# Kernel tuning notes

Hardware: AMD Instinct MI355X
Metric: run time of the kernel (lower is better)

The kernel has to match this reference:

```python
import jax, jax.numpy as jnp
import numpy as np

N_NODES = 100000
N_EDGES = 640000


def _sage_conv(x, src, dst, w_agg, b, w_root, n_nodes):
    # mean aggregation of source features into destination nodes
    msgs = x[src]  # [E, D] gather
    summed = jax.ops.segment_sum(msgs, dst, num_segments=n_nodes)  # [N, D]
    deg = jax.ops.segment_sum(jnp.ones((src.shape[0],), dtype=x.dtype), dst,
                              num_segments=n_nodes)  # [N]
    mean = summed / jnp.clip(deg, 1.0)[:, None]  # isolated nodes -> 0
    # PyG SAGEConv: lin_l(agg) + lin_r(x); bias lives on lin_l
    return mean @ w_agg.T + b + x @ w_root.T


def setup_inputs() -> dict:
    key = jax.random.key(0)
    ks = jax.random.split(key, 8)
    d_in, d_hid, d_out = 128, 256, 64
    x = jax.random.normal(ks[0], (N_NODES, d_in), dtype=jnp.float32)
    edge_index = jax.random.randint(ks[1], (2, N_EDGES), 0, N_NODES, dtype=jnp.int64)
    s = 0.05
    return {
        "x": x,
        "edge_index": edge_index,
        "w1_agg": jax.random.normal(ks[2], (d_hid, d_in), dtype=jnp.float32) * s,
        "b1": jax.random.normal(ks[3], (d_hid,), dtype=jnp.float32) * s,
        "w1_root": jax.random.normal(ks[4], (d_hid, d_in), dtype=jnp.float32) * s,
        "w2_agg": jax.random.normal(ks[5], (d_out, d_hid), dtype=jnp.float32) * s,
        "b2": jax.random.normal(ks[6], (d_out,), dtype=jnp.float32) * s,
        "w2_root": jax.random.normal(ks[7], (d_out, d_hid), dtype=jnp.float32) * s,
    }


def reference(x, edge_index, w1_agg, b1, w1_root, w2_agg, b2, w2_root):
    src, dst = edge_index[0], edge_index[1]
    n = x.shape[0]
    h = _sage_conv(x, src, dst, w1_agg, b1, w1_root, n)
    h = jax.nn.relu(h)
    # dropout(p=0.5) is identity in eval mode
    h = _sage_conv(h, src, dst, w2_agg, b2, w2_root, n)
    return jax.nn.log_softmax(h, axis=1)
```

## Files before the change

### kernel.cpp

```cpp
#include <hip/hip_runtime.h>

#define N_NODES 100000
#define N_EDGES 640000
#define D_IN 128
#define D_HID 256
#define D_OUT 64

#define NROWPAD 100096
#define CAP 32

#define OB_CNT      0u
#define OB_BUCKET   401408u
#define OB_XB       13201408u
#define OB_XQ       38825984u
#define OB_MEANB    51638272u
#define OB_HB       77262848u
#define OB_ZRB      128512000u
#define OB_ZAQ      141324288u
#define OB_WCAT1    147730432u
#define OB_WCAT2    147861504u

typedef __attribute__((ext_vector_type(8))) short bf16x8;
typedef __attribute__((ext_vector_type(8))) ushort ushort8;
typedef __attribute__((ext_vector_type(4))) float f32x4;
typedef __attribute__((ext_vector_type(2))) float f32x2;

__device__ __forceinline__ ushort f2bf(float f) {
    uint u = __float_as_uint(f);
    u += 0x7FFFu + ((u >> 16) & 1u);
    return (ushort)(u >> 16);
}
__device__ __forceinline__ float bf1(ushort u) { return __uint_as_float((uint)u << 16); }
__device__ __forceinline__ uchar f2q(float v) {
    return (uchar)(__builtin_amdgcn_cvt_pk_fp8_f32(v, v, 0, false) & 0xFF);
}
__device__ __forceinline__ uint pk8(float4 v) {
    uint q = (uint)__builtin_amdgcn_cvt_pk_fp8_f32(v.x, v.y, 0, false);
    return (uint)__builtin_amdgcn_cvt_pk_fp8_f32(v.z, v.w, (int)q, true);
}


__global__ __launch_bounds__(256) void k_z(
    int* __restrict__ cnt,
    const float* __restrict__ w1a, const float* __restrict__ w1r,
    const float* __restrict__ w2r, const float* __restrict__ w2a,
    ushort* __restrict__ wcat1, ushort* __restrict__ wcat2)
{
    int b = blockIdx.x;
    if (b < 98) {
        int i = (b * 256 + threadIdx.x) * 4;
        *(int4*)(cnt + i) = make_int4(0, 0, 0, 0);
    } else {
        int i = (b - 98) * 256 + threadIdx.x;
        if (i < 65536) {
            int n = i >> 8, k = i & 255;
            float v = (k < 128) ? w1a[n * 128 + k] : w1r[n * 128 + (k - 128)];
            wcat1[i] = f2bf(v);
        } else {
            int j = i - 65536;
            int n = j >> 8, k = j & 255;
            float v = (n < 64) ? w2r[n * 256 + k] : w2a[(n - 64) * 256 + k];
            wcat2[j] = f2bf(v);
        }
    }
}


__global__ __launch_bounds__(256) void k_fc(
    const int* __restrict__ src, const int* __restrict__ dst,
    int* __restrict__ cnt, int* __restrict__ bucket,
    const float* __restrict__ x, ushort* __restrict__ xb,
    uchar* __restrict__ xq)
{
    int b = blockIdx.x;
    if (b < 625) {
        int e = (b * 256 + threadIdx.x) * 4;
        int4 d = *(const int4*)(dst + e);
        int4 sv = *(const int4*)(src + e);
        int p0 = atomicAdd(&cnt[d.x], 1);
        int p1 = atomicAdd(&cnt[d.y], 1);
        int p2 = atomicAdd(&cnt[d.z], 1);
        int p3 = atomicAdd(&cnt[d.w], 1);
        if (p0 < CAP) bucket[(d.x << 5) + p0] = sv.x;
        if (p1 < CAP) bucket[(d.y << 5) + p1] = sv.y;
        if (p2 < CAP) bucket[(d.z << 5) + p2] = sv.z;
        if (p3 < CAP) bucket[(d.w << 5) + p3] = sv.w;
    } else {
        size_t i = ((size_t)(b - 625) * 256 + threadIdx.x) * 16;
        float4 v0 = *(const float4*)(x + i);
        float4 v1 = *(const float4*)(x + i + 4);
        float4 v2 = *(const float4*)(x + i + 8);
        float4 v3 = *(const float4*)(x + i + 12);
        ushort8 o0, o1;
        o0[0]=f2bf(v0.x); o0[1]=f2bf(v0.y); o0[2]=f2bf(v0.z); o0[3]=f2bf(v0.w);
        o0[4]=f2bf(v1.x); o0[5]=f2bf(v1.y); o0[6]=f2bf(v1.z); o0[7]=f2bf(v1.w);
        o1[0]=f2bf(v2.x); o1[1]=f2bf(v2.y); o1[2]=f2bf(v2.z); o1[3]=f2bf(v2.w);
        o1[4]=f2bf(v3.x); o1[5]=f2bf(v3.y); o1[6]=f2bf(v3.z); o1[7]=f2bf(v3.w);
        *(ushort8*)(xb + i) = o0;
        *(ushort8*)(xb + i + 8) = o1;
        uint4 q;
        q.x = pk8(v0); q.y = pk8(v1); q.z = pk8(v2); q.w = pk8(v3);
        *(uint4*)(xq + i) = q;
    }
}


__global__ __launch_bounds__(256) void k_gather(
    const uchar* __restrict__ xq, const int* __restrict__ cnt,
    const int* __restrict__ bucket, ushort* __restrict__ meanb)
{
    int tid = threadIdx.x;
    int node = blockIdx.x * 8 + (tid >> 5);
    int l = tid & 31;
    int g = l & 3, t = l >> 2;
    int nraw = cnt[node];
    int n = min(nraw, CAP);
    const int* cs = bucket + (node << 5);

    float a[16] = {};
    for (int j = 0; j < n; j += 4) {
        int jj = j + g;
        int ii = (jj < n) ? jj : 0;
        float w = (jj < n) ? 1.0f : 0.0f;
        int s = cs[ii];
        uint4 q = *(const uint4*)(xq + (size_t)s * D_IN + t * 16);
        f32x2 p;
        p = __builtin_amdgcn_cvt_pk_f32_fp8(q.x, false); a[0] += w*p.x; a[1] += w*p.y;
        p = __builtin_amdgcn_cvt_pk_f32_fp8(q.x, true);  a[2] += w*p.x; a[3] += w*p.y;
        p = __builtin_amdgcn_cvt_pk_f32_fp8(q.y, false); a[4] += w*p.x; a[5] += w*p.y;
        p = __builtin_amdgcn_cvt_pk_f32_fp8(q.y, true);  a[6] += w*p.x; a[7] += w*p.y;
        p = __builtin_amdgcn_cvt_pk_f32_fp8(q.z, false); a[8] += w*p.x; a[9] += w*p.y;
        p = __builtin_amdgcn_cvt_pk_f32_fp8(q.z, true);  a[10]+= w*p.x; a[11]+= w*p.y;
        p = __builtin_amdgcn_cvt_pk_f32_fp8(q.w, false); a[12]+= w*p.x; a[13]+= w*p.y;
        p = __builtin_amdgcn_cvt_pk_f32_fp8(q.w, true);  a[14]+= w*p.x; a[15]+= w*p.y;
    }

    float b[8];
    #pragma unroll
    for (int j = 0; j < 8; ++j) {
        int base = (j & 3) + 8 * (j >> 2);
        float mine = (l & 1) ? a[base + 4] : a[base];
        float send = (l & 1) ? a[base]     : a[base + 4];
        b[j] = mine + __shfl_xor(send, 1);
    }
    float c[4];
    #pragma unroll
    for (int j = 0; j < 4; ++j) {
        float mine = (l & 2) ? b[j + 4] : b[j];
        float send = (l & 2) ? b[j]     : b[j + 4];
        c[j] = mine + __shfl_xor(send, 2);
    }
    float id = 1.0f / fmaxf((float)nraw, 1.0f);
    ushort4 o;
    o.x = f2bf(c[0] * id); o.y = f2bf(c[1] * id);
    o.z = f2bf(c[2] * id); o.w = f2bf(c[3] * id);
    *(ushort4*)(meanb + (size_t)node * D_IN + t * 16 + (l & 3) * 4) = o;
}


template<int AW, int MODE>
__global__ __launch_bounds__(256, 2) void k_gemm(
    const ushort* __restrict__ A0, const ushort* __restrict__ A1,
    const ushort* __restrict__ B,
    const float* __restrict__ bias,
    void* __restrict__ out0, void* __restrict__ out1)
{
    __shared__ ushort lds[2 * 128 * 64];

    const int tid = threadIdx.x;
    const int lane = tid & 63;
    const int w = tid >> 6;
    const int wm = w >> 1, wn = w & 1;
    const int row0 = blockIdx.x * 128;
    const int col0 = blockIdx.y * 128;

    f32x4 acc[4][4] = {};

    for (int kt = 0; kt < 4; ++kt) {
        const int k0 = kt * 64;
        const ushort* asrc;
        int kofs;
        if (AW == 256) { asrc = A0; kofs = k0; }
        else { asrc = (k0 < 128) ? A0 : A1; kofs = k0 & 127; }

        #pragma unroll
        for (int i = 0; i < 4; ++i) {
            int elem = i * 256 + tid;
            int r = elem >> 3;
            int c8 = (elem & 7) ^ (r & 7);
            const ushort* g = asrc + (size_t)(row0 + r) * AW + kofs + c8 * 8;
            __builtin_amdgcn_global_load_lds(
                (const __attribute__((address_space(1))) void*)g,
                (__attribute__((address_space(3))) void*)&lds[i * 2048 + w * 512],
                16, 0, 0);
        }
        #pragma unroll
        for (int i = 0; i < 4; ++i) {
            int elem = i * 256 + tid;
            int r = elem >> 3;
            int c8 = (elem & 7) ^ (r & 7);
            const ushort* g = B + (size_t)(col0 + r) * 256 + k0 + c8 * 8;
            __builtin_amdgcn_global_load_lds(
                (const __attribute__((address_space(1))) void*)g,
                (__attribute__((address_space(3))) void*)&lds[8192 + i * 2048 + w * 512],
                16, 0, 0);
        }
        asm volatile("s_waitcnt vmcnt(0)" ::: "memory");
        __syncthreads();

        #pragma unroll
        for (int ks = 0; ks < 2; ++ks) {
            bf16x8 af[4], bfr[4];
            #pragma unroll
            for (int mi = 0; mi < 4; ++mi) {
                int r = wm * 64 + mi * 16 + (lane & 15);
                int c8 = ks * 4 + (lane >> 4);
                int byteoff = r * 128 + ((c8 ^ (r & 7)) * 16);
                af[mi] = *(const bf16x8*)((const char*)lds + byteoff);
            }
            #pragma unroll
            for (int ni = 0; ni < 4; ++ni) {
                int r = wn * 64 + ni * 16 + (lane & 15);
                int c8 = ks * 4 + (lane >> 4);
                int byteoff = 16384 + r * 128 + ((c8 ^ (r & 7)) * 16);
                bfr[ni] = *(const bf16x8*)((const char*)lds + byteoff);
            }
            #pragma unroll
            for (int mi = 0; mi < 4; ++mi)
                #pragma unroll
                for (int ni = 0; ni < 4; ++ni)
                    acc[mi][ni] = __builtin_amdgcn_mfma_f32_16x16x32_bf16(
                        af[mi], bfr[ni], acc[mi][ni], 0, 0, 0);
        }
        __syncthreads();
    }

    const int orow_base = row0 + wm * 64;
    const int ocol_base = col0 + wn * 64;
    #pragma unroll
    for (int mi = 0; mi < 4; ++mi) {
        #pragma unroll
        for (int ni = 0; ni < 4; ++ni) {
            int ocol = ocol_base + ni * 16 + (lane & 15);
            #pragma unroll
            for (int r = 0; r < 4; ++r) {
                int orow = orow_base + mi * 16 + (lane >> 4) * 4 + r;
                float v = acc[mi][ni][r];
                if (MODE == 0) {
                    v = fmaxf(v + bias[ocol], 0.0f);
                    ((ushort*)out0)[(size_t)orow * 256 + ocol] = f2bf(v);
                } else {
                    if (ocol < 64)
                        ((ushort*)out0)[(size_t)orow * 64 + ocol] = f2bf(v + bias[ocol]);
                    else
                        ((uchar*)out1)[(size_t)orow * 64 + (ocol - 64)] = f2q(v);
                }
            }
        }
    }
}


__global__ __launch_bounds__(256) void k_final(
    const ushort* __restrict__ zrb, const uchar* __restrict__ zaq,
    const int* __restrict__ cnt, const int* __restrict__ bucket,
    float* __restrict__ out)
{
    int tid = threadIdx.x;
    int lane = tid & 63;
    int l = lane & 31;
    int node = blockIdx.x * 8 + (tid >> 5);
    int g = l & 7, t = l >> 3;
    int nraw = cnt[node];
    int n = min(nraw, CAP);
    const int* cs = bucket + (node << 5);

    float a[16] = {};
    for (int j = 0; j < n; j += 8) {
        int jj = j + g;
        int ii = (jj < n) ? jj : 0;
        float w = (jj < n) ? 1.0f : 0.0f;
        int s = cs[ii];
        uint4 q = *(const uint4*)(zaq + (size_t)s * 64 + t * 16);
        f32x2 p;
        p = __builtin_amdgcn_cvt_pk_f32_fp8(q.x, false); a[0] += w*p.x; a[1] += w*p.y;
        p = __builtin_amdgcn_cvt_pk_f32_fp8(q.x, true);  a[2] += w*p.x; a[3] += w*p.y;
        p = __builtin_amdgcn_cvt_pk_f32_fp8(q.y, false); a[4] += w*p.x; a[5] += w*p.y;
        p = __builtin_amdgcn_cvt_pk_f32_fp8(q.y, true);  a[6] += w*p.x; a[7] += w*p.y;
        p = __builtin_amdgcn_cvt_pk_f32_fp8(q.z, false); a[8] += w*p.x; a[9] += w*p.y;
        p = __builtin_amdgcn_cvt_pk_f32_fp8(q.z, true);  a[10]+= w*p.x; a[11]+= w*p.y;
        p = __builtin_amdgcn_cvt_pk_f32_fp8(q.w, false); a[12]+= w*p.x; a[13]+= w*p.y;
        p = __builtin_amdgcn_cvt_pk_f32_fp8(q.w, true);  a[14]+= w*p.x; a[15]+= w*p.y;
    }

    float b[8];
    #pragma unroll
    for (int j = 0; j < 8; ++j) {
        float mine = (l & 1) ? a[2*j+1] : a[2*j];
        float send = (l & 1) ? a[2*j]   : a[2*j+1];
        b[j] = mine + __shfl_xor(send, 1);
    }
    float c[4];
    #pragma unroll
    for (int j = 0; j < 4; ++j) {
        float mine = (l & 2) ? b[2*j+1] : b[2*j];
        float send = (l & 2) ? b[2*j]   : b[2*j+1];
        c[j] = mine + __shfl_xor(send, 2);
    }
    float m0 = (l & 4) ? c[1] : c[0];
    float s0 = (l & 4) ? c[0] : c[1];
    float e0 = m0 + __shfl_xor(s0, 4);
    float m1 = (l & 4) ? c[3] : c[2];
    float s1 = (l & 4) ? c[2] : c[3];
    float e1 = m1 + __shfl_xor(s1, 4);

    int c0 = t * 16 + (l & 7);
    float id = 1.0f / fmaxf((float)nraw, 1.0f);
    float v0 = e0 * id + bf1(zrb[(size_t)node * 64 + c0]);
    float v1 = e1 * id + bf1(zrb[(size_t)node * 64 + c0 + 8]);

    float m = fmaxf(v0, v1);
    #pragma unroll
    for (int o = 1; o < 32; o <<= 1) m = fmaxf(m, __shfl_xor(m, o));
    float ssum = __expf(v0 - m) + __expf(v1 - m);
    #pragma unroll
    for (int o = 1; o < 32; o <<= 1) ssum += __shfl_xor(ssum, o);
    float lse = m + __logf(ssum);

    out[(size_t)node * 64 + c0]     = v0 - lse;
    out[(size_t)node * 64 + c0 + 8] = v1 - lse;
}


extern "C" void kernel_launch(void* const* d_in, const int* in_sizes, int n_in,
                              void* d_out, int out_size, void* d_ws, size_t ws_size,
                              hipStream_t stream)
{
    const float* x   = (const float*)d_in[0];
    const int*   ei  = (const int*)d_in[1];
    const float* w1a = (const float*)d_in[2];
    const float* b1  = (const float*)d_in[3];
    const float* w1r = (const float*)d_in[4];
    const float* w2a = (const float*)d_in[5];
    const float* b2  = (const float*)d_in[6];
    const float* w2r = (const float*)d_in[7];
    float* out = (float*)d_out;

    char* ws = (char*)d_ws;
    const int* src = ei;
    const int* dst = ei + N_EDGES;

    int*    cnt       = (int*)(ws + OB_CNT);
    int*    bucket    = (int*)(ws + OB_BUCKET);
    ushort* xb        = (ushort*)(ws + OB_XB);
    uchar*  xq        = (uchar*)(ws + OB_XQ);
    ushort* meanb     = (ushort*)(ws + OB_MEANB);
    ushort* hb        = (ushort*)(ws + OB_HB);
    ushort* zrb       = (ushort*)(ws + OB_ZRB);
    uchar*  zaq       = (uchar*)(ws + OB_ZAQ);
    ushort* wcat1     = (ushort*)(ws + OB_WCAT1);
    ushort* wcat2     = (ushort*)(ws + OB_WCAT2);

    k_z<<<482, 256, 0, stream>>>(cnt, w1a, w1r, w2r, w2a, wcat1, wcat2);
    k_fc<<<3750, 256, 0, stream>>>(src, dst, cnt, bucket, x, xb, xq);

    k_gather<<<12500, 256, 0, stream>>>(xq, cnt, bucket, meanb);

    dim3 g1(NROWPAD / 128, 2);
    k_gemm<128, 0><<<g1, 256, 0, stream>>>(meanb, xb, wcat1, b1, (void*)hb, nullptr);

    dim3 g2(NROWPAD / 128, 1);
    k_gemm<256, 1><<<g2, 256, 0, stream>>>(hb, hb, wcat2, b2, (void*)zrb, (void*)zaq);

    k_final<<<12500, 256, 0, stream>>>(zrb, zaq, cnt, bucket, out);
}
```

Before: 157.0 us.

## Store layer-1 GEMM A operands as fp8 and dequantize to bf16 in LDS reads

Drops the bf16 copy of x and stores the aggregated mean as fp8 instead of bf16. The layer-1 GEMM now loads fp8 A tiles into LDS with a 4-chunk swizzle and converts them to bf16 in registers before the MFMA. This halves the A-operand bytes written and read, and removes one full-size write of x. In exchange it adds conversion ALU work in the GEMM inner loop and loses precision on the root-term input and the mean.

```diff
diff --git a/kernel.cpp b/kernel.cpp
--- a/kernel.cpp
+++ b/kernel.cpp
@@ -11,17 +11,15 @@
 
 #define OB_CNT      0u
 #define OB_BUCKET   401408u
-#define OB_XB       13201408u
-#define OB_XQ       38825984u
-#define OB_MEANB    51638272u
-#define OB_HB       77262848u
-#define OB_ZRB      128512000u
-#define OB_ZAQ      141324288u
-#define OB_WCAT1    147730432u
-#define OB_WCAT2    147861504u
+#define OB_XQ       13201408u
+#define OB_MEANQ    26013696u
+#define OB_HB       38825984u
+#define OB_ZRB      90075136u
+#define OB_ZAQ      102887424u
+#define OB_WCAT1    109293568u
+#define OB_WCAT2    109424640u
 
 typedef __attribute__((ext_vector_type(8))) short bf16x8;
-typedef __attribute__((ext_vector_type(8))) ushort ushort8;
 typedef __attribute__((ext_vector_type(4))) float f32x4;
 typedef __attribute__((ext_vector_type(2))) float f32x2;
 
@@ -37,6 +35,9 @@
 __device__ __forceinline__ uint pk8(float4 v) {
     uint q = (uint)__builtin_amdgcn_cvt_pk_fp8_f32(v.x, v.y, 0, false);
     return (uint)__builtin_amdgcn_cvt_pk_fp8_f32(v.z, v.w, (int)q, true);
+}
+__device__ __forceinline__ uint pkbf(float lo, float hi) {
+    return (__float_as_uint(lo) >> 16) | (__float_as_uint(hi) & 0xFFFF0000u);
 }
 
 
@@ -69,8 +70,7 @@
 __global__ __launch_bounds__(256) void k_fc(
     const int* __restrict__ src, const int* __restrict__ dst,
     int* __restrict__ cnt, int* __restrict__ bucket,
-    const float* __restrict__ x, ushort* __restrict__ xb,
-    uchar* __restrict__ xq)
+    const float* __restrict__ x, uchar* __restrict__ xq)
 {
     int b = blockIdx.x;
     if (b < 625) {
@@ -91,13 +91,6 @@
         float4 v1 = *(const float4*)(x + i + 4);
         float4 v2 = *(const float4*)(x + i + 8);
         float4 v3 = *(const float4*)(x + i + 12);
-        ushort8 o0, o1;
-        o0[0]=f2bf(v0.x); o0[1]=f2bf(v0.y); o0[2]=f2bf(v0.z); o0[3]=f2bf(v0.w);
-        o0[4]=f2bf(v1.x); o0[5]=f2bf(v1.y); o0[6]=f2bf(v1.z); o0[7]=f2bf(v1.w);
-        o1[0]=f2bf(v2.x); o1[1]=f2bf(v2.y); o1[2]=f2bf(v2.z); o1[3]=f2bf(v2.w);
-        o1[4]=f2bf(v3.x); o1[5]=f2bf(v3.y); o1[6]=f2bf(v3.z); o1[7]=f2bf(v3.w);
-        *(ushort8*)(xb + i) = o0;
-        *(ushort8*)(xb + i + 8) = o1;
         uint4 q;
         q.x = pk8(v0); q.y = pk8(v1); q.z = pk8(v2); q.w = pk8(v3);
         *(uint4*)(xq + i) = q;
@@ -107,7 +100,7 @@
 
 __global__ __launch_bounds__(256) void k_gather(
     const uchar* __restrict__ xq, const int* __restrict__ cnt,
-    const int* __restrict__ bucket, ushort* __restrict__ meanb)
+    const int* __restrict__ bucket, uchar* __restrict__ meanq)
 {
     int tid = threadIdx.x;
     int node = blockIdx.x * 8 + (tid >> 5);
@@ -151,21 +144,21 @@
         c[j] = mine + __shfl_xor(send, 2);
     }
     float id = 1.0f / fmaxf((float)nraw, 1.0f);
-    ushort4 o;
-    o.x = f2bf(c[0] * id); o.y = f2bf(c[1] * id);
-    o.z = f2bf(c[2] * id); o.w = f2bf(c[3] * id);
-    *(ushort4*)(meanb + (size_t)node * D_IN + t * 16 + (l & 3) * 4) = o;
-}
-
-
-template<int AW, int MODE>
+    uint q = (uint)__builtin_amdgcn_cvt_pk_fp8_f32(c[0] * id, c[1] * id, 0, false);
+    q = (uint)__builtin_amdgcn_cvt_pk_fp8_f32(c[2] * id, c[3] * id, (int)q, true);
+    *(uint*)(meanq + (size_t)node * D_IN + t * 16 + (l & 3) * 4) = q;
+}
+
+
+template<int MODE>
 __global__ __launch_bounds__(256, 2) void k_gemm(
-    const ushort* __restrict__ A0, const ushort* __restrict__ A1,
+    const void* __restrict__ A0v, const void* __restrict__ A1v,
     const ushort* __restrict__ B,
     const float* __restrict__ bias,
     void* __restrict__ out0, void* __restrict__ out1)
 {
-    __shared__ ushort lds[2 * 128 * 64];
+    __shared__ char lds[32 * 1024];
+    const int BB = (MODE == 0) ? 8192 : 16384;
 
     const int tid = threadIdx.x;
     const int lane = tid & 63;
@@ -178,31 +171,44 @@
 
     for (int kt = 0; kt < 4; ++kt) {
         const int k0 = kt * 64;
-        const ushort* asrc;
-        int kofs;
-        if (AW == 256) { asrc = A0; kofs = k0; }
-        else { asrc = (k0 < 128) ? A0 : A1; kofs = k0 & 127; }
-
+
+        if (MODE == 0) {
+            const uchar* asrc = (kt < 2) ? (const uchar*)A0v : (const uchar*)A1v;
+            int kbyte = (kt & 1) * 64;
+            #pragma unroll
+            for (int i = 0; i < 2; ++i) {
+                int elem = i * 256 + tid;
+                int r = elem >> 2;
+                int c4 = (elem & 3) ^ (r & 3);
+                const uchar* gp = asrc + (size_t)(row0 + r) * 128 + kbyte + c4 * 16;
+                __builtin_amdgcn_global_load_lds(
+                    (const __attribute__((address_space(1))) void*)gp,
+                    (__attribute__((address_space(3))) void*)&lds[i * 4096 + w * 1024],
+                    16, 0, 0);
+            }
+        } else {
+            const ushort* asrc = (const ushort*)A0v;
+            #pragma unroll
+            for (int i = 0; i < 4; ++i) {
+                int elem = i * 256 + tid;
+                int r = elem >> 3;
+                int c8 = (elem & 7) ^ (r & 7);
+                const ushort* gp = asrc + (size_t)(row0 + r) * 256 + k0 + c8 * 8;
+                __builtin_amdgcn_global_load_lds(
+                    (const __attribute__((address_space(1))) void*)gp,
+                    (__attribute__((address_space(3))) void*)&lds[i * 4096 + w * 1024],
+                    16, 0, 0);
+            }
+        }
         #pragma unroll
         for (int i = 0; i < 4; ++i) {
             int elem = i * 256 + tid;
             int r = elem >> 3;
             int c8 = (elem & 7) ^ (r & 7);
-            const ushort* g = asrc + (size_t)(row0 + r) * AW + kofs + c8 * 8;
+            const ushort* gp = B + (size_t)(col0 + r) * 256 + k0 + c8 * 8;
             __builtin_amdgcn_global_load_lds(
-                (const __attribute__((address_space(1))) void*)g,
-                (__attribute__((address_space(3))) void*)&lds[i * 2048 + w * 512],
-                16, 0, 0);
-        }
-        #pragma unroll
-        for (int i = 0; i < 4; ++i) {
-            int elem = i * 256 + tid;
-            int r = elem >> 3;
-            int c8 = (elem & 7) ^ (r & 7);
-            const ushort* g = B + (size_t)(col0 + r) * 256 + k0 + c8 * 8;
-            __builtin_amdgcn_global_load_lds(
-                (const __attribute__((address_space(1))) void*)g,
-                (__attribute__((address_space(3))) void*)&lds[8192 + i * 2048 + w * 512],
+                (const __attribute__((address_space(1))) void*)gp,
+                (__attribute__((address_space(3))) void*)&lds[BB + i * 4096 + w * 1024],
                 16, 0, 0);
         }
         asm volatile("s_waitcnt vmcnt(0)" ::: "memory");
@@ -214,16 +220,31 @@
             #pragma unroll
             for (int mi = 0; mi < 4; ++mi) {
                 int r = wm * 64 + mi * 16 + (lane & 15);
-                int c8 = ks * 4 + (lane >> 4);
-                int byteoff = r * 128 + ((c8 ^ (r & 7)) * 16);
-                af[mi] = *(const bf16x8*)((const char*)lds + byteoff);
+                int g = lane >> 4;
+                if (MODE == 0) {
+                    int c4l = ks * 2 + (g >> 1);
+                    int abyte = r * 64 + ((c4l ^ (r & 3)) << 4) + ((g & 1) << 3);
+                    uint2 q = *(const uint2*)(lds + abyte);
+                    f32x2 p0 = __builtin_amdgcn_cvt_pk_f32_fp8(q.x, false);
+                    f32x2 p1 = __builtin_amdgcn_cvt_pk_f32_fp8(q.x, true);
+                    f32x2 p2 = __builtin_amdgcn_cvt_pk_f32_fp8(q.y, false);
+                    f32x2 p3 = __builtin_amdgcn_cvt_pk_f32_fp8(q.y, true);
+                    uint4 u;
+                    u.x = pkbf(p0.x, p0.y); u.y = pkbf(p1.x, p1.y);
+                    u.z = pkbf(p2.x, p2.y); u.w = pkbf(p3.x, p3.y);
+                    af[mi] = *(bf16x8*)&u;
+                } else {
+                    int c8 = ks * 4 + g;
+                    int abyte = r * 128 + ((c8 ^ (r & 7)) << 4);
+                    af[mi] = *(const bf16x8*)(lds + abyte);
+                }
             }
             #pragma unroll
             for (int ni = 0; ni < 4; ++ni) {
                 int r = wn * 64 + ni * 16 + (lane & 15);
                 int c8 = ks * 4 + (lane >> 4);
-                int byteoff = 16384 + r * 128 + ((c8 ^ (r & 7)) * 16);
-                bfr[ni] = *(const bf16x8*)((const char*)lds + byteoff);
+                int byteoff = BB + r * 128 + ((c8 ^ (r & 7)) << 4);
+                bfr[ni] = *(const bf16x8*)(lds + byteoff);
             }
             #pragma unroll
             for (int mi = 0; mi < 4; ++mi)
@@ -352,9 +373,8 @@
 
     int*    cnt       = (int*)(ws + OB_CNT);
     int*    bucket    = (int*)(ws + OB_BUCKET);
-    ushort* xb        = (ushort*)(ws + OB_XB);
     uchar*  xq        = (uchar*)(ws + OB_XQ);
-    ushort* meanb     = (ushort*)(ws + OB_MEANB);
+    uchar*  meanq     = (uchar*)(ws + OB_MEANQ);
     ushort* hb        = (ushort*)(ws + OB_HB);
     ushort* zrb       = (ushort*)(ws + OB_ZRB);
     uchar*  zaq       = (uchar*)(ws + OB_ZAQ);
@@ -362,15 +382,17 @@
     ushort* wcat2     = (ushort*)(ws + OB_WCAT2);
 
     k_z<<<482, 256, 0, stream>>>(cnt, w1a, w1r, w2r, w2a, wcat1, wcat2);
-    k_fc<<<3750, 256, 0, stream>>>(src, dst, cnt, bucket, x, xb, xq);
-
-    k_gather<<<12500, 256, 0, stream>>>(xq, cnt, bucket, meanb);
+    k_fc<<<3750, 256, 0, stream>>>(src, dst, cnt, bucket, x, xq);
+
+    k_gather<<<12500, 256, 0, stream>>>(xq, cnt, bucket, meanq);
 
     dim3 g1(NROWPAD / 128, 2);
-    k_gemm<128, 0><<<g1, 256, 0, stream>>>(meanb, xb, wcat1, b1, (void*)hb, nullptr);
+    k_gemm<0><<<g1, 256, 0, stream>>>((const void*)meanq, (const void*)xq,
+                                      wcat1, b1, (void*)hb, nullptr);
 
     dim3 g2(NROWPAD / 128, 1);
-    k_gemm<256, 1><<<g2, 256, 0, stream>>>(hb, hb, wcat2, b2, (void*)zrb, (void*)zaq);
+    k_gemm<1><<<g2, 256, 0, stream>>>((const void*)hb, (const void*)hb,
+                                      wcat2, b2, (void*)zrb, (void*)zaq);
 
     k_final<<<12500, 256, 0, stream>>>(zrb, zaq, cnt, bucket, out);
 }
```

Result: faster. 147.7 us (-5.9%).
